# Performance work log

Hardware: AMD Instinct MI355X
Metric: run time of the kernel (lower is better)

Reference implementation:

```python
import jax, jax.numpy as jnp
import numpy as np

N = 100000   # number of vertices
E = 20000    # number of hyperedges
NNZ = 1000000  # incidence entries
D = 64
ALPHA = 0.5
BETA = 0.5


def setup_inputs() -> dict:
    key = jax.random.key(0)
    ks = jax.random.split(key, 8)
    s = 1.0 / np.sqrt(D)
    return {
        "X": jax.random.normal(ks[0], (N, D), dtype=jnp.float32),
        "X0": jax.random.normal(ks[1], (N, D), dtype=jnp.float32),
        "W1": jax.random.normal(ks[2], (D, D), dtype=jnp.float32) * s,
        "b1": jnp.zeros((D,), dtype=jnp.float32),
        "W2": jax.random.normal(ks[3], (D, D), dtype=jnp.float32) * s,
        "b2": jnp.zeros((D,), dtype=jnp.float32),
        "vertex": jax.random.randint(ks[4], (NNZ,), 0, N),
        "edges": jax.random.randint(ks[5], (NNZ,), 0, E),
    }


def reference(X, X0, W1, b1, W2, b2, vertex, edges):
    # vertex -> edge aggregation (scatter-add)
    Xve = X[vertex]                                    # [nnz, D]
    Xe = jax.ops.segment_sum(Xve, edges, num_segments=E)   # [E, D]
    # edge -> vertex aggregation
    Xev = Xe[edges]                                    # [nnz, D]
    Xv = jax.ops.segment_sum(Xev, vertex, num_segments=N)  # [N, D]
    # jump link residual + MLP
    Xi = (1.0 - ALPHA) * Xv + ALPHA * X0
    h = jax.nn.relu(Xi @ W1 + b1)
    mlp = h @ W2 + b2
    return (1.0 - BETA) * Xi + BETA * mlp
```

## Files before the change

kernel.cpp:

```cpp
#include <hip/hip_runtime.h>

#define NV    100000
#define NE    20000
#define NNZT  1000000
#define DIM   64

#define EBITS 4
#define ELOC  16
#define EBK   (NE / ELOC)
#define CAP_E 1024
#define ESH   17
#define EMASK 0x1FFFF

#define VBITS 6
#define VLOC  64
#define VBK   ((NV + VLOC - 1) / VLOC)
#define CAP_V 896
#define VSH   15
#define VMASK 0x7FFF

#define CHUNK 4096
#define NBIN  ((NNZT + CHUNK - 1) / CHUNK)

#define MROWS 128

__global__ __launch_bounds__(256) void bin_kernel(
    const int* __restrict__ vertex, const int* __restrict__ edges,
    int* __restrict__ ecur, int* __restrict__ vcur,
    unsigned int* __restrict__ erecs, unsigned int* __restrict__ vrecs) {
    __shared__ int hE[EBK], hV[VBK];
    __shared__ int cE[EBK], cV[VBK];
    int tid = threadIdx.x;
    for (int t = tid; t < EBK; t += 256) hE[t] = 0;
    for (int t = tid; t < VBK; t += 256) hV[t] = 0;
    __syncthreads();
    int base4 = blockIdx.x * (CHUNK / 4);
    #pragma unroll
    for (int k = 0; k < CHUNK / 4 / 256; k++) {
        int i = base4 + k * 256 + tid;
        if (i < NNZT / 4) {
            int4 e = ((const int4*)edges)[i];
            int4 v = ((const int4*)vertex)[i];
            atomicAdd(&hE[e.x >> EBITS], 1); atomicAdd(&hE[e.y >> EBITS], 1);
            atomicAdd(&hE[e.z >> EBITS], 1); atomicAdd(&hE[e.w >> EBITS], 1);
            atomicAdd(&hV[v.x >> VBITS], 1); atomicAdd(&hV[v.y >> VBITS], 1);
            atomicAdd(&hV[v.z >> VBITS], 1); atomicAdd(&hV[v.w >> VBITS], 1);
        }
    }
    __syncthreads();
    for (int t = tid; t < EBK; t += 256) { int h = hE[t]; cE[t] = h ? atomicAdd(&ecur[t], h) : 0; }
    for (int t = tid; t < VBK; t += 256) { int h = hV[t]; cV[t] = h ? atomicAdd(&vcur[t], h) : 0; }
    __syncthreads();
    #pragma unroll
    for (int k = 0; k < CHUNK / 4 / 256; k++) {
        int i = base4 + k * 256 + tid;
        if (i < NNZT / 4) {
            int4 e = ((const int4*)edges)[i];
            int4 v = ((const int4*)vertex)[i];
            int be, bv, p;
            be = e.x >> EBITS; p = atomicAdd(&cE[be], 1); if (p < CAP_E) erecs[be * CAP_E + p] = ((unsigned)(e.x & 15) << ESH) | (unsigned)v.x;
            be = e.y >> EBITS; p = atomicAdd(&cE[be], 1); if (p < CAP_E) erecs[be * CAP_E + p] = ((unsigned)(e.y & 15) << ESH) | (unsigned)v.y;
            be = e.z >> EBITS; p = atomicAdd(&cE[be], 1); if (p < CAP_E) erecs[be * CAP_E + p] = ((unsigned)(e.z & 15) << ESH) | (unsigned)v.z;
            be = e.w >> EBITS; p = atomicAdd(&cE[be], 1); if (p < CAP_E) erecs[be * CAP_E + p] = ((unsigned)(e.w & 15) << ESH) | (unsigned)v.w;
            bv = v.x >> VBITS; p = atomicAdd(&cV[bv], 1); if (p < CAP_V) vrecs[bv * CAP_V + p] = ((unsigned)(v.x & 63) << VSH) | (unsigned)e.x;
            bv = v.y >> VBITS; p = atomicAdd(&cV[bv], 1); if (p < CAP_V) vrecs[bv * CAP_V + p] = ((unsigned)(v.y & 63) << VSH) | (unsigned)e.y;
            bv = v.z >> VBITS; p = atomicAdd(&cV[bv], 1); if (p < CAP_V) vrecs[bv * CAP_V + p] = ((unsigned)(v.z & 63) << VSH) | (unsigned)e.z;
            bv = v.w >> VBITS; p = atomicAdd(&cV[bv], 1); if (p < CAP_V) vrecs[bv * CAP_V + p] = ((unsigned)(v.w & 63) << VSH) | (unsigned)e.w;
        }
    }
}

__global__ __launch_bounds__(256, 4) void agg_edges_srt(
    const float* __restrict__ X,
    const int* __restrict__ ebc, const unsigned int* __restrict__ erecs,
    float* __restrict__ Xe) {
    __shared__ int rbuf[CAP_E];
    __shared__ int sbuf[CAP_E];
    __shared__ int boff[ELOC + 1];
    __shared__ int bcur[ELOC];
    int tid = threadIdx.x;
    int b = blockIdx.x;
    int cnt = ebc[b]; if (cnt > CAP_E) cnt = CAP_E;
    const unsigned int* src = erecs + (size_t)b * CAP_E;
    for (int t = tid; t < cnt; t += 256) rbuf[t] = (int)src[t];
    if (tid < ELOC) bcur[tid] = 0;
    __syncthreads();
    for (int t = tid; t < cnt; t += 256) atomicAdd(&bcur[((unsigned)rbuf[t]) >> ESH], 1);
    __syncthreads();
    if (tid == 0) {
        int run = 0;
        for (int i = 0; i < ELOC; i++) { int c = bcur[i]; boff[i] = run; bcur[i] = run; run += c; }
        boff[ELOC] = run;
    }
    __syncthreads();
    for (int t = tid; t < cnt; t += 256) {
        unsigned r = (unsigned)rbuf[t];
        int p = atomicAdd(&bcur[r >> ESH], 1);
        sbuf[p] = (int)(r & EMASK);
    }
    __syncthreads();

    int wave = tid >> 6, lane = tid & 63;
    #pragma unroll
    for (int q = 0; q < 4; q++) {
        int le = wave * 4 + q;
        int beg = boff[le], end = boff[le + 1];
        float acc = 0.f;
        int j = beg;
        for (; j + 8 <= end; j += 8) {
            int v0 = sbuf[j],     v1 = sbuf[j + 1], v2 = sbuf[j + 2], v3 = sbuf[j + 3];
            int v4 = sbuf[j + 4], v5 = sbuf[j + 5], v6 = sbuf[j + 6], v7 = sbuf[j + 7];
            float a0 = X[v0 * DIM + lane], a1 = X[v1 * DIM + lane];
            float a2 = X[v2 * DIM + lane], a3 = X[v3 * DIM + lane];
            float a4 = X[v4 * DIM + lane], a5 = X[v5 * DIM + lane];
            float a6 = X[v6 * DIM + lane], a7 = X[v7 * DIM + lane];
            acc += ((a0 + a1) + (a2 + a3)) + ((a4 + a5) + (a6 + a7));
        }
        for (; j + 4 <= end; j += 4) {
            int v0 = sbuf[j], v1 = sbuf[j + 1], v2 = sbuf[j + 2], v3 = sbuf[j + 3];
            float a0 = X[v0 * DIM + lane], a1 = X[v1 * DIM + lane];
            float a2 = X[v2 * DIM + lane], a3 = X[v3 * DIM + lane];
            acc += (a0 + a1) + (a2 + a3);
        }
        for (; j < end; j++) acc += X[sbuf[j] * DIM + lane];
        Xe[(size_t)(b * ELOC + le) * DIM + lane] = acc;
    }
}

__global__ __launch_bounds__(256) void agg_verts_srt(
    const float* __restrict__ Xe, const float* __restrict__ X0,
    const int* __restrict__ vbc, const unsigned int* __restrict__ vrecs,
    float* __restrict__ xi_out) {
    __shared__ int rbuf[CAP_V];
    __shared__ int sbuf[CAP_V];
    __shared__ int boff[VLOC + 1];
    __shared__ int bcur[VLOC];
    int tid = threadIdx.x;
    int b = blockIdx.x;
    int cnt = vbc[b]; if (cnt > CAP_V) cnt = CAP_V;
    const unsigned int* src = vrecs + (size_t)b * CAP_V;
    for (int t = tid; t < cnt; t += 256) rbuf[t] = (int)src[t];
    if (tid < VLOC) bcur[tid] = 0;
    __syncthreads();
    for (int t = tid; t < cnt; t += 256) atomicAdd(&bcur[((unsigned)rbuf[t]) >> VSH], 1);
    __syncthreads();
    if (tid == 0) {
        int run = 0;
        for (int i = 0; i < VLOC; i++) { int c = bcur[i]; boff[i] = run; bcur[i] = run; run += c; }
        boff[VLOC] = run;
    }
    __syncthreads();
    for (int t = tid; t < cnt; t += 256) {
        unsigned r = (unsigned)rbuf[t];
        int p = atomicAdd(&bcur[r >> VSH], 1);
        sbuf[p] = (int)(r & VMASK);
    }
    __syncthreads();

    int wave = tid >> 6, lane = tid & 63;
    int row0 = b << VBITS;
    for (int q = 0; q < 16; q++) {
        int lv = wave * 16 + q;
        int row = row0 + lv;
        if (row >= NV) break;
        int beg = boff[lv], end = boff[lv + 1];
        float acc = 0.f;
        int j = beg;
        for (; j + 8 <= end; j += 8) {
            int e0 = sbuf[j],     e1 = sbuf[j + 1], e2 = sbuf[j + 2], e3 = sbuf[j + 3];
            int e4 = sbuf[j + 4], e5 = sbuf[j + 5], e6 = sbuf[j + 6], e7 = sbuf[j + 7];
            float a0 = Xe[e0 * DIM + lane], a1 = Xe[e1 * DIM + lane];
            float a2 = Xe[e2 * DIM + lane], a3 = Xe[e3 * DIM + lane];
            float a4 = Xe[e4 * DIM + lane], a5 = Xe[e5 * DIM + lane];
            float a6 = Xe[e6 * DIM + lane], a7 = Xe[e7 * DIM + lane];
            acc += ((a0 + a1) + (a2 + a3)) + ((a4 + a5) + (a6 + a7));
        }
        for (; j + 4 <= end; j += 4) {
            int e0 = sbuf[j], e1 = sbuf[j + 1], e2 = sbuf[j + 2], e3 = sbuf[j + 3];
            float a0 = Xe[e0 * DIM + lane], a1 = Xe[e1 * DIM + lane];
            float a2 = Xe[e2 * DIM + lane], a3 = Xe[e3 * DIM + lane];
            acc += (a0 + a1) + (a2 + a3);
        }
        for (; j < end; j++) acc += Xe[sbuf[j] * DIM + lane];
        float xi = 0.5f * acc + 0.5f * X0[(size_t)row * DIM + lane];
        xi_out[(size_t)row * DIM + lane] = xi;
    }
}

__device__ __forceinline__ void fma4x4(float4& h, const float4 x,
                                       const float4 w0, const float4 w1,
                                       const float4 w2, const float4 w3) {
    h.x = fmaf(x.x, w0.x, fmaf(x.y, w1.x, fmaf(x.z, w2.x, fmaf(x.w, w3.x, h.x))));
    h.y = fmaf(x.x, w0.y, fmaf(x.y, w1.y, fmaf(x.z, w2.y, fmaf(x.w, w3.y, h.y))));
    h.z = fmaf(x.x, w0.z, fmaf(x.y, w1.z, fmaf(x.z, w2.z, fmaf(x.w, w3.z, h.z))));
    h.w = fmaf(x.x, w0.w, fmaf(x.y, w1.w, fmaf(x.z, w2.w, fmaf(x.w, w3.w, h.w))));
}

__global__ __launch_bounds__(256) void mlp_kernel(
    const float* __restrict__ W1, const float* __restrict__ b1,
    const float* __restrict__ W2, const float* __restrict__ b2,
    float* __restrict__ io) {
    __shared__ float sW[DIM * DIM];
    __shared__ float ht[MROWS * DIM];
    int tid = threadIdx.x;
    for (int t = tid; t < DIM * DIM / 4; t += 256) ((float4*)sW)[t] = ((const float4*)W1)[t];
    __syncthreads();

    int rgq = tid >> 4, cgi = tid & 15;
    int row0 = blockIdx.x * MROWS + rgq * 8;
    const float4* w4 = (const float4*)sW;
    const float4* io4 = (const float4*)io;
    float4* ht4 = (float4*)ht;

    float4 bias1 = ((const float4*)b1)[cgi];
    float4 h[8];
    #pragma unroll
    for (int r = 0; r < 8; r++) h[r] = bias1;
    #pragma unroll 2
    for (int k = 0; k < DIM; k += 4) {
        float4 w0 = w4[(k + 0) * 16 + cgi];
        float4 w1v = w4[(k + 1) * 16 + cgi];
        float4 w2v = w4[(k + 2) * 16 + cgi];
        float4 w3v = w4[(k + 3) * 16 + cgi];
        #pragma unroll
        for (int r = 0; r < 8; r++) {
            int row = row0 + r;
            float4 x = (row < NV) ? io4[(size_t)row * 16 + (k >> 2)]
                                  : make_float4(0.f, 0.f, 0.f, 0.f);
            fma4x4(h[r], x, w0, w1v, w2v, w3v);
        }
    }
    #pragma unroll
    for (int r = 0; r < 8; r++) {
        float4 v = h[r];
        v.x = fmaxf(v.x, 0.f); v.y = fmaxf(v.y, 0.f);
        v.z = fmaxf(v.z, 0.f); v.w = fmaxf(v.w, 0.f);
        ht4[(rgq * 8 + r) * 16 + cgi] = v;
    }
    __syncthreads();
    for (int t = tid; t < DIM * DIM / 4; t += 256) ((float4*)sW)[t] = ((const float4*)W2)[t];
    __syncthreads();

    float4 bias2 = ((const float4*)b2)[cgi];
    float4 m[8];
    #pragma unroll
    for (int r = 0; r < 8; r++) m[r] = bias2;
    #pragma unroll 2
    for (int k = 0; k < DIM; k += 4) {
        float4 w0 = w4[(k + 0) * 16 + cgi];
        float4 w1v = w4[(k + 1) * 16 + cgi];
        float4 w2v = w4[(k + 2) * 16 + cgi];
        float4 w3v = w4[(k + 3) * 16 + cgi];
        #pragma unroll
        for (int r = 0; r < 8; r++) {
            float4 x = ht4[(rgq * 8 + r) * 16 + (k >> 2)];
            fma4x4(m[r], x, w0, w1v, w2v, w3v);
        }
    }
    #pragma unroll
    for (int r = 0; r < 8; r++) {
        int row = row0 + r;
        if (row < NV) {
            float4 xi = io4[(size_t)row * 16 + cgi];
            float4 o;
            o.x = 0.5f * xi.x + 0.5f * m[r].x;
            o.y = 0.5f * xi.y + 0.5f * m[r].y;
            o.z = 0.5f * xi.z + 0.5f * m[r].z;
            o.w = 0.5f * xi.w + 0.5f * m[r].w;
            ((float4*)io)[(size_t)row * 16 + cgi] = o;
        }
    }
}

extern "C" void kernel_launch(void* const* d_in, const int* in_sizes, int n_in,
                              void* d_out, int out_size, void* d_ws, size_t ws_size,
                              hipStream_t stream) {
    const float* X  = (const float*)d_in[0];
    const float* X0 = (const float*)d_in[1];
    const float* W1 = (const float*)d_in[2];
    const float* b1 = (const float*)d_in[3];
    const float* W2 = (const float*)d_in[4];
    const float* b2 = (const float*)d_in[5];
    const int* vertex = (const int*)d_in[6];
    const int* edges  = (const int*)d_in[7];
    float* out = (float*)d_out;

    int* ecur = (int*)d_ws;
    int* vcur = ecur + EBK;
    unsigned int* erecs = (unsigned int*)(vcur + VBK);
    unsigned int* vrecs = erecs + (size_t)EBK * CAP_E;
    float* Xe = (float*)(vrecs + (size_t)VBK * CAP_V);

    hipMemsetAsync(d_ws, 0, (size_t)(EBK + VBK) * sizeof(int), stream);

    dim3 blk(256);
    bin_kernel<<<NBIN, blk, 0, stream>>>(vertex, edges, ecur, vcur, erecs, vrecs);
    agg_edges_srt<<<EBK, blk, 0, stream>>>(X, ecur, erecs, Xe);
    agg_verts_srt<<<VBK, blk, 0, stream>>>(Xe, X0, vcur, vrecs, out);
    mlp_kernel<<<(NV + MROWS - 1) / MROWS, blk, 0, stream>>>(W1, b1, W2, b2, out);
}
```

Before: 267.6 us.

## Store edge features in bf16 and run MLP on bf16 MFMA

Edge aggregates Xe are now written as bf16, which halves the gather traffic in the edge-to-vertex aggregation. The MLP is rewritten to use 16x16x32 bf16 MFMA instructions, with transposed bf16 weights produced by a small new conversion kernel. This replaces the scalar fp32 FMA GEMM. The cost is reduced precision in both the aggregation and the MLP, plus one extra tiny kernel launch. The new MLP also reads its A operand with strided scalar loads and writes output element by element, so those accesses are not coalesced.

```diff
diff --git a/kernel.cpp b/kernel.cpp
--- a/kernel.cpp
+++ b/kernel.cpp
@@ -22,7 +22,17 @@
 #define CHUNK 4096
 #define NBIN  ((NNZT + CHUNK - 1) / CHUNK)
 
-#define MROWS 128
+typedef __attribute__((ext_vector_type(8))) short bf16x8;
+typedef __attribute__((ext_vector_type(4))) float f32x4;
+
+__device__ __forceinline__ float bf2f(unsigned short u) {
+    return __uint_as_float(((unsigned)u) << 16);
+}
+__device__ __forceinline__ unsigned short f2bf(float f) {
+    unsigned u = __float_as_uint(f);
+    u += 0x7FFF + ((u >> 16) & 1);
+    return (unsigned short)(u >> 16);
+}
 
 __global__ __launch_bounds__(256) void bin_kernel(
     const int* __restrict__ vertex, const int* __restrict__ edges,
@@ -70,10 +80,21 @@
     }
 }
 
+__global__ __launch_bounds__(256) void conv_w(
+    const float* __restrict__ W1, const float* __restrict__ W2,
+    unsigned short* __restrict__ W1T, unsigned short* __restrict__ W2T) {
+    int tid = threadIdx.x;
+    for (int t = tid; t < DIM * DIM; t += 256) {
+        int k = t >> 6, n = t & 63;
+        W1T[n * DIM + k] = f2bf(W1[k * DIM + n]);
+        W2T[n * DIM + k] = f2bf(W2[k * DIM + n]);
+    }
+}
+
 __global__ __launch_bounds__(256, 4) void agg_edges_srt(
     const float* __restrict__ X,
     const int* __restrict__ ebc, const unsigned int* __restrict__ erecs,
-    float* __restrict__ Xe) {
+    unsigned short* __restrict__ Xeb) {
     __shared__ int rbuf[CAP_E];
     __shared__ int sbuf[CAP_E];
     __shared__ int boff[ELOC + 1];
@@ -123,12 +144,12 @@
             acc += (a0 + a1) + (a2 + a3);
         }
         for (; j < end; j++) acc += X[sbuf[j] * DIM + lane];
-        Xe[(size_t)(b * ELOC + le) * DIM + lane] = acc;
+        Xeb[(size_t)(b * ELOC + le) * DIM + lane] = f2bf(acc);
     }
 }
 
 __global__ __launch_bounds__(256) void agg_verts_srt(
-    const float* __restrict__ Xe, const float* __restrict__ X0,
+    const unsigned short* __restrict__ Xeb, const float* __restrict__ X0,
     const int* __restrict__ vbc, const unsigned int* __restrict__ vrecs,
     float* __restrict__ xi_out) {
     __shared__ int rbuf[CAP_V];
@@ -169,105 +190,100 @@
         for (; j + 8 <= end; j += 8) {
             int e0 = sbuf[j],     e1 = sbuf[j + 1], e2 = sbuf[j + 2], e3 = sbuf[j + 3];
             int e4 = sbuf[j + 4], e5 = sbuf[j + 5], e6 = sbuf[j + 6], e7 = sbuf[j + 7];
-            float a0 = Xe[e0 * DIM + lane], a1 = Xe[e1 * DIM + lane];
-            float a2 = Xe[e2 * DIM + lane], a3 = Xe[e3 * DIM + lane];
-            float a4 = Xe[e4 * DIM + lane], a5 = Xe[e5 * DIM + lane];
-            float a6 = Xe[e6 * DIM + lane], a7 = Xe[e7 * DIM + lane];
+            float a0 = bf2f(Xeb[e0 * DIM + lane]), a1 = bf2f(Xeb[e1 * DIM + lane]);
+            float a2 = bf2f(Xeb[e2 * DIM + lane]), a3 = bf2f(Xeb[e3 * DIM + lane]);
+            float a4 = bf2f(Xeb[e4 * DIM + lane]), a5 = bf2f(Xeb[e5 * DIM + lane]);
+            float a6 = bf2f(Xeb[e6 * DIM + lane]), a7 = bf2f(Xeb[e7 * DIM + lane]);
             acc += ((a0 + a1) + (a2 + a3)) + ((a4 + a5) + (a6 + a7));
         }
         for (; j + 4 <= end; j += 4) {
             int e0 = sbuf[j], e1 = sbuf[j + 1], e2 = sbuf[j + 2], e3 = sbuf[j + 3];
-            float a0 = Xe[e0 * DIM + lane], a1 = Xe[e1 * DIM + lane];
-            float a2 = Xe[e2 * DIM + lane], a3 = Xe[e3 * DIM + lane];
+            float a0 = bf2f(Xeb[e0 * DIM + lane]), a1 = bf2f(Xeb[e1 * DIM + lane]);
+            float a2 = bf2f(Xeb[e2 * DIM + lane]), a3 = bf2f(Xeb[e3 * DIM + lane]);
             acc += (a0 + a1) + (a2 + a3);
         }
-        for (; j < end; j++) acc += Xe[sbuf[j] * DIM + lane];
+        for (; j < end; j++) acc += bf2f(Xeb[sbuf[j] * DIM + lane]);
         float xi = 0.5f * acc + 0.5f * X0[(size_t)row * DIM + lane];
         xi_out[(size_t)row * DIM + lane] = xi;
     }
 }
 
-__device__ __forceinline__ void fma4x4(float4& h, const float4 x,
-                                       const float4 w0, const float4 w1,
-                                       const float4 w2, const float4 w3) {
-    h.x = fmaf(x.x, w0.x, fmaf(x.y, w1.x, fmaf(x.z, w2.x, fmaf(x.w, w3.x, h.x))));
-    h.y = fmaf(x.x, w0.y, fmaf(x.y, w1.y, fmaf(x.z, w2.y, fmaf(x.w, w3.y, h.y))));
-    h.z = fmaf(x.x, w0.z, fmaf(x.y, w1.z, fmaf(x.z, w2.z, fmaf(x.w, w3.z, h.z))));
-    h.w = fmaf(x.x, w0.w, fmaf(x.y, w1.w, fmaf(x.z, w2.w, fmaf(x.w, w3.w, h.w))));
-}
-
-__global__ __launch_bounds__(256) void mlp_kernel(
-    const float* __restrict__ W1, const float* __restrict__ b1,
-    const float* __restrict__ W2, const float* __restrict__ b2,
+__global__ __launch_bounds__(256) void mlp_mfma(
+    const unsigned short* __restrict__ W1T, const unsigned short* __restrict__ W2T,
+    const float* __restrict__ b1, const float* __restrict__ b2,
     float* __restrict__ io) {
-    __shared__ float sW[DIM * DIM];
-    __shared__ float ht[MROWS * DIM];
-    int tid = threadIdx.x;
-    for (int t = tid; t < DIM * DIM / 4; t += 256) ((float4*)sW)[t] = ((const float4*)W1)[t];
-    __syncthreads();
-
-    int rgq = tid >> 4, cgi = tid & 15;
-    int row0 = blockIdx.x * MROWS + rgq * 8;
-    const float4* w4 = (const float4*)sW;
-    const float4* io4 = (const float4*)io;
-    float4* ht4 = (float4*)ht;
-
-    float4 bias1 = ((const float4*)b1)[cgi];
-    float4 h[8];
-    #pragma unroll
-    for (int r = 0; r < 8; r++) h[r] = bias1;
-    #pragma unroll 2
-    for (int k = 0; k < DIM; k += 4) {
-        float4 w0 = w4[(k + 0) * 16 + cgi];
-        float4 w1v = w4[(k + 1) * 16 + cgi];
-        float4 w2v = w4[(k + 2) * 16 + cgi];
-        float4 w3v = w4[(k + 3) * 16 + cgi];
+    __shared__ __align__(16) unsigned short sW1[DIM * DIM];
+    __shared__ __align__(16) unsigned short sW2[DIM * DIM];
+    __shared__ __align__(16) unsigned short ht[4][16 * 72];
+    int tid = threadIdx.x;
+    for (int t = tid; t < DIM * DIM / 8; t += 256) {
+        ((bf16x8*)sW1)[t] = ((const bf16x8*)W1T)[t];
+        ((bf16x8*)sW2)[t] = ((const bf16x8*)W2T)[t];
+    }
+    __syncthreads();
+
+    int wave = tid >> 6, lane = tid & 63;
+    int m = lane & 15, quad = lane >> 4;
+    int row0 = blockIdx.x * 64 + wave * 16;
+
+    int arow = row0 + m;
+    bool avalid = (arow < NV);
+    const float* xrow = io + (size_t)(avalid ? arow : 0) * DIM;
+    bf16x8 a0, a1;
+    #pragma unroll
+    for (int j = 0; j < 8; j++) {
+        float x0 = avalid ? xrow[quad * 8 + j] : 0.f;
+        float x1 = avalid ? xrow[32 + quad * 8 + j] : 0.f;
+        a0[j] = (short)f2bf(x0);
+        a1[j] = (short)f2bf(x1);
+    }
+
+    f32x4 h[4];
+    #pragma unroll
+    for (int nt = 0; nt < 4; nt++) {
+        float bias = b1[nt * 16 + m];
+        f32x4 c = {bias, bias, bias, bias};
+        const bf16x8* wb = (const bf16x8*)(sW1 + (nt * 16 + m) * DIM);
+        c = __builtin_amdgcn_mfma_f32_16x16x32_bf16(a0, wb[quad], c, 0, 0, 0);
+        c = __builtin_amdgcn_mfma_f32_16x16x32_bf16(a1, wb[4 + quad], c, 0, 0, 0);
+        h[nt] = c;
+    }
+
+    unsigned short* hw = ht[wave];
+    #pragma unroll
+    for (int nt = 0; nt < 4; nt++) {
         #pragma unroll
-        for (int r = 0; r < 8; r++) {
-            int row = row0 + r;
-            float4 x = (row < NV) ? io4[(size_t)row * 16 + (k >> 2)]
-                                  : make_float4(0.f, 0.f, 0.f, 0.f);
-            fma4x4(h[r], x, w0, w1v, w2v, w3v);
-        }
-    }
-    #pragma unroll
-    for (int r = 0; r < 8; r++) {
-        float4 v = h[r];
-        v.x = fmaxf(v.x, 0.f); v.y = fmaxf(v.y, 0.f);
-        v.z = fmaxf(v.z, 0.f); v.w = fmaxf(v.w, 0.f);
-        ht4[(rgq * 8 + r) * 16 + cgi] = v;
-    }
-    __syncthreads();
-    for (int t = tid; t < DIM * DIM / 4; t += 256) ((float4*)sW)[t] = ((const float4*)W2)[t];
-    __syncthreads();
-
-    float4 bias2 = ((const float4*)b2)[cgi];
-    float4 m[8];
-    #pragma unroll
-    for (int r = 0; r < 8; r++) m[r] = bias2;
-    #pragma unroll 2
-    for (int k = 0; k < DIM; k += 4) {
-        float4 w0 = w4[(k + 0) * 16 + cgi];
-        float4 w1v = w4[(k + 1) * 16 + cgi];
-        float4 w2v = w4[(k + 2) * 16 + cgi];
-        float4 w3v = w4[(k + 3) * 16 + cgi];
+        for (int r = 0; r < 4; r++) {
+            float v = fmaxf(h[nt][r], 0.f);
+            hw[(quad * 4 + r) * 72 + nt * 16 + m] = f2bf(v);
+        }
+    }
+    __syncthreads();
+
+    bf16x8 g0 = *(const bf16x8*)(hw + m * 72 + quad * 8);
+    bf16x8 g1 = *(const bf16x8*)(hw + m * 72 + 32 + quad * 8);
+
+    f32x4 o[4];
+    #pragma unroll
+    for (int nt = 0; nt < 4; nt++) {
+        float bias = b2[nt * 16 + m];
+        f32x4 c = {bias, bias, bias, bias};
+        const bf16x8* wb = (const bf16x8*)(sW2 + (nt * 16 + m) * DIM);
+        c = __builtin_amdgcn_mfma_f32_16x16x32_bf16(g0, wb[quad], c, 0, 0, 0);
+        c = __builtin_amdgcn_mfma_f32_16x16x32_bf16(g1, wb[4 + quad], c, 0, 0, 0);
+        o[nt] = c;
+    }
+
+    #pragma unroll
+    for (int nt = 0; nt < 4; nt++) {
         #pragma unroll
-        for (int r = 0; r < 8; r++) {
-            float4 x = ht4[(rgq * 8 + r) * 16 + (k >> 2)];
-            fma4x4(m[r], x, w0, w1v, w2v, w3v);
-        }
-    }
-    #pragma unroll
-    for (int r = 0; r < 8; r++) {
-        int row = row0 + r;
-        if (row < NV) {
-            float4 xi = io4[(size_t)row * 16 + cgi];
-            float4 o;
-            o.x = 0.5f * xi.x + 0.5f * m[r].x;
-            o.y = 0.5f * xi.y + 0.5f * m[r].y;
-            o.z = 0.5f * xi.z + 0.5f * m[r].z;
-            o.w = 0.5f * xi.w + 0.5f * m[r].w;
-            ((float4*)io)[(size_t)row * 16 + cgi] = o;
+        for (int r = 0; r < 4; r++) {
+            int row = row0 + quad * 4 + r;
+            if (row < NV) {
+                size_t idx = (size_t)row * DIM + nt * 16 + m;
+                float xi = io[idx];
+                io[idx] = 0.5f * xi + 0.5f * o[nt][r];
+            }
         }
     }
 }
@@ -285,17 +301,22 @@
     const int* edges  = (const int*)d_in[7];
     float* out = (float*)d_out;
 
-    int* ecur = (int*)d_ws;
-    int* vcur = ecur + EBK;
-    unsigned int* erecs = (unsigned int*)(vcur + VBK);
-    unsigned int* vrecs = erecs + (size_t)EBK * CAP_E;
-    float* Xe = (float*)(vrecs + (size_t)VBK * CAP_V);
+    char* p = (char*)d_ws;
+    int* ecur = (int*)p;                          p += (size_t)EBK * 4;
+    int* vcur = (int*)p;                          p += (size_t)VBK * 4;
+    p = (char*)(((uintptr_t)p + 15) & ~(uintptr_t)15);
+    unsigned int* erecs = (unsigned int*)p;       p += (size_t)EBK * CAP_E * 4;
+    unsigned int* vrecs = (unsigned int*)p;       p += (size_t)VBK * CAP_V * 4;
+    unsigned short* Xeb = (unsigned short*)p;     p += (size_t)NE * DIM * 2;
+    unsigned short* W1T = (unsigned short*)p;     p += (size_t)DIM * DIM * 2;
+    unsigned short* W2T = (unsigned short*)p;     p += (size_t)DIM * DIM * 2;
 
     hipMemsetAsync(d_ws, 0, (size_t)(EBK + VBK) * sizeof(int), stream);
 
     dim3 blk(256);
     bin_kernel<<<NBIN, blk, 0, stream>>>(vertex, edges, ecur, vcur, erecs, vrecs);
-    agg_edges_srt<<<EBK, blk, 0, stream>>>(X, ecur, erecs, Xe);
-    agg_verts_srt<<<VBK, blk, 0, stream>>>(Xe, X0, vcur, vrecs, out);
-    mlp_kernel<<<(NV + MROWS - 1) / MROWS, blk, 0, stream>>>(W1, b1, W2, b2, out);
-}
+    conv_w<<<1, blk, 0, stream>>>(W1, W2, W1T, W2T);
+    agg_edges_srt<<<EBK, blk, 0, stream>>>(X, ecur, erecs, Xeb);
+    agg_verts_srt<<<VBK, blk, 0, stream>>>(Xeb, X0, vcur, vrecs, out);
+    mlp_mfma<<<(NV + 63) / 64, blk, 0, stream>>>(W1T, W2T, b1, b2, out);
+}
```

New measurement: 233.8 us. -12.6%, faster.
